# Performance work log

Measured on AMD Instinct MI355X. Metric: run time of the kernel, lower is better.

The kernel has to match this reference:

```python
import jax, jax.numpy as jnp
import numpy as np

B, T, D, H = 2, 2048, 1024, 16
DK = D // H


def setup_inputs() -> dict:
    key = jax.random.key(0)
    ks = jax.random.split(key, 13)
    s = 1.0 / np.sqrt(D)
    return {
        "q": jax.random.normal(ks[0], (B, T, D), jnp.float32),
        "k": jax.random.normal(ks[1], (B, T, D), jnp.float32),
        "v": jax.random.normal(ks[2], (B, T, D), jnp.float32),
        "mask": jax.random.randint(ks[3], (B, T, T), 0, 2, jnp.int32),
        "Wq": jax.random.normal(ks[4], (D, D), jnp.float32) * s,
        "bq": jax.random.normal(ks[5], (D,), jnp.float32) * s,
        "Wk": jax.random.normal(ks[6], (D, D), jnp.float32) * s,
        "bk": jax.random.normal(ks[7], (D,), jnp.float32) * s,
        "Wv": jax.random.normal(ks[8], (D, D), jnp.float32) * s,
        "bv": jax.random.normal(ks[9], (D,), jnp.float32) * s,
        "Wo": jax.random.normal(ks[10], (D, D), jnp.float32) * s,
        "bo": jax.random.normal(ks[11], (D,), jnp.float32) * s,
    }


def reference(q, k, v, mask, Wq, bq, Wk, bk, Wv, bv, Wo, bo):
    # Linear projections (torch Linear: x @ W.T + b), split into heads.
    Q = (q @ Wq.T + bq).reshape(B, T, H, DK).transpose(0, 2, 1, 3)  # [B,H,Tq,dk]
    K = (k @ Wk.T + bk).reshape(B, T, H, DK).transpose(0, 2, 1, 3)
    V = (v @ Wv.T + bv).reshape(B, T, H, DK).transpose(0, 2, 1, 3)
    scores = jnp.einsum("bhqd,bhkd->bhqk", Q, K) / jnp.sqrt(jnp.float32(DK))
    # 3-dim mask path: mask==0 -> -1e9, broadcast over heads.
    scores = jnp.where(mask[:, None, :, :] == 0, jnp.float32(-1e9), scores)
    attn = jax.nn.softmax(scores, axis=-1)
    out = jnp.einsum("bhqk,bhkd->bhqd", attn, V)  # [B,H,Tq,dk]
    out = out.transpose(0, 2, 1, 3).reshape(B, T, D)
    return out @ Wo.T + bo
```

## Files before the change

kernel.cpp:

```cpp
#include <hip/hip_runtime.h>
#include <cstdint>
#include <cstddef>

#define TSEQ 2048
#define DMOD 1024
#define NHEAD 16
#define NBATCH 2
#define MT (NBATCH * TSEQ)
#define LOG2E 1.44269504088896340736f

typedef __attribute__((ext_vector_type(8))) __bf16 bf16x8;
typedef __attribute__((ext_vector_type(4))) float f32x4;
typedef __attribute__((ext_vector_type(8))) unsigned short u16x8;
typedef __attribute__((ext_vector_type(4))) unsigned short u16x4;
typedef __attribute__((ext_vector_type(4))) uint32_t u32x4;

__device__ __forceinline__ unsigned short f2bf(float f) {
  uint32_t u = __builtin_bit_cast(uint32_t, f);
  u += 0x7fffu + ((u >> 16) & 1u);
  return (unsigned short)(u >> 16);
}

__device__ __forceinline__ uint32_t cvt_pk_bf16(float a, float b) {
  uint32_t r;
  asm("v_cvt_pk_bf16_f32 %0, %1, %2" : "=v"(r) : "v"(a), "v"(b));
  return r;
}

__device__ __forceinline__ void gload_lds16(const void* g, const void* l) {
  auto gp = (const __attribute__((address_space(1))) uint32_t*)((uintptr_t)g);
  auto lp = (__attribute__((address_space(3))) uint32_t*)((uintptr_t)l);
  __builtin_amdgcn_global_load_lds(gp, lp, 16, 0, 0);
}

__global__ __launch_bounds__(256) void cvt_all(const float* __restrict__ q,
                                               const float* __restrict__ k,
                                               const float* __restrict__ v,
                                               const float* __restrict__ w0,
                                               const float* __restrict__ w1,
                                               const float* __restrict__ w2,
                                               const float* __restrict__ w3,
                                               unsigned short* __restrict__ din,
                                               unsigned short* __restrict__ dw) {
  const int y = blockIdx.y;
  const float* s;
  unsigned short* d;
  size_t n;
  if (y < 3) {
    s = y == 0 ? q : (y == 1 ? k : v);
    d = din + (size_t)y * MT * DMOD;
    n = (size_t)MT * DMOD;
  } else {
    s = y == 3 ? w0 : (y == 4 ? w1 : (y == 5 ? w2 : w3));
    d = dw + (size_t)(y - 3) * DMOD * DMOD;
    n = (size_t)DMOD * DMOD;
  }
  const size_t i = ((size_t)blockIdx.x * 256 + threadIdx.x) * 4;
  if (i >= n) return;
  const float4 t = *(const float4*)(s + i);
  u16x4 o;
  o[0] = f2bf(t.x); o[1] = f2bf(t.y); o[2] = f2bf(t.z); o[3] = f2bf(t.w);
  *(u16x4*)(d + i) = o;
}

__global__ __launch_bounds__(256) void mask_exp(const int* __restrict__ m,
                                                uint32_t* __restrict__ mx) {
  const size_t W = (size_t)blockIdx.x * 256 + threadIdx.x;
  const int hi = (int)((W >> 3) & 3), ct = (int)(W & 7);
  const size_t bqkt = W >> 5;
  const int kt = (int)(bqkt & 15);
  const size_t bq = bqkt >> 4;
  const int4 mm = *(const int4*)(m + bq * TSEQ + kt * 128 + ct * 16 + hi * 4);
  const uint32_t o = (mm.x ? 0xFFu : 0u) | (mm.y ? 0xFF00u : 0u) |
                     (mm.z ? 0xFF0000u : 0u) | (mm.w ? 0xFF000000u : 0u);
  mx[W] = o;
}

__device__ __forceinline__ void store_c(unsigned short* C, size_t idx, float v) { C[idx] = f2bf(v); }
__device__ __forceinline__ void store_c(float* C, size_t idx, float v) { C[idx] = v; }

template <typename OT, int MF>
__global__ __launch_bounds__(256) void gemm_bt(const unsigned short* __restrict__ A0,
                                               const unsigned short* __restrict__ A1,
                                               const unsigned short* __restrict__ A2,
                                               const unsigned short* __restrict__ W0,
                                               const unsigned short* __restrict__ W1,
                                               const unsigned short* __restrict__ W2,
                                               const float* __restrict__ b0,
                                               const float* __restrict__ b1,
                                               const float* __restrict__ b2,
                                               OT* __restrict__ C0, OT* __restrict__ C1, OT* __restrict__ C2,
                                               float s0, float s1, float s2) {
  constexpr int BM = MF * 32;
  const int z = blockIdx.z;
  const unsigned short* A  = z == 0 ? A0 : (z == 1 ? A1 : A2);
  const unsigned short* Bw = z == 0 ? W0 : (z == 1 ? W1 : W2);
  const float* bias = z == 0 ? b0 : (z == 1 ? b1 : b2);
  OT* C = z == 0 ? C0 : (z == 1 ? C1 : C2);
  const float scale = z == 0 ? s0 : (z == 1 ? s1 : s2);

  __shared__ alignas(16) unsigned short As[BM * 32];
  __shared__ alignas(16) unsigned short Bs[128 * 32];
  const int tid = threadIdx.x;
  const int wid = tid >> 6;
  const int lane = tid & 63;
  const int lo = lane & 15, hi = lane >> 4;
  const int m0 = blockIdx.x * BM, n0 = blockIdx.y * 128;
  const int wr = wid >> 1, wc = wid & 1;
  f32x4 acc[MF][4] = {};

  for (int k0 = 0; k0 < DMOD; k0 += 32) {
    __syncthreads();
#pragma unroll
    for (int i = 0; i < 2; ++i) {
      const int chunk = i * 256 + tid;
      const int row = chunk >> 2, c = chunk & 3;
      const int wb = (i * 256 + wid * 64) * 16;
      if (i < MF / 2)
        gload_lds16(A + (size_t)(m0 + row) * DMOD + k0 + c * 8, (const char*)As + wb);
      gload_lds16(Bw + (size_t)(n0 + row) * DMOD + k0 + c * 8, (const char*)Bs + wb);
    }
    __syncthreads();
    bf16x8 af[MF], bfr[4];
#pragma unroll
    for (int m = 0; m < MF; ++m)
      af[m] = *(const bf16x8*)((const char*)As + (wr * (MF * 16) + m * 16 + lo) * 64 + hi * 16);
#pragma unroll
    for (int n = 0; n < 4; ++n)
      bfr[n] = *(const bf16x8*)((const char*)Bs + (wc * 64 + n * 16 + lo) * 64 + hi * 16);
#pragma unroll
    for (int m = 0; m < MF; ++m)
#pragma unroll
      for (int n = 0; n < 4; ++n)
        acc[m][n] = __builtin_amdgcn_mfma_f32_16x16x32_bf16(af[m], bfr[n], acc[m][n], 0, 0, 0);
  }

#pragma unroll
  for (int n = 0; n < 4; ++n) {
    const int col = n0 + wc * 64 + n * 16 + lo;
    const float bv = bias[col];
#pragma unroll
    for (int m = 0; m < MF; ++m) {
      const int row = m0 + wr * (MF * 16) + m * 16 + hi * 4;
#pragma unroll
      for (int r = 0; r < 4; ++r)
        store_c(C, (size_t)(row + r) * DMOD + col, (acc[m][n][r] + bv) * scale);
    }
  }
}

__global__ __launch_bounds__(256) void transpose_v(const unsigned short* __restrict__ Vp,
                                                   unsigned short* __restrict__ Vt) {
  __shared__ alignas(16) unsigned short tile[64][72];
  const int tid = threadIdx.x;
  const int bt0 = blockIdx.x * 64;
  const int h = blockIdx.y;
  const int b = bt0 >> 11;
  const int t0 = bt0 & (TSEQ - 1);
#pragma unroll
  for (int i = 0; i < 2; ++i) {
    const int chunk = i * 256 + tid;
    const int row = chunk >> 3, c = chunk & 7;
    *(uint4*)((char*)&tile[row][0] + c * 16) =
        *(const uint4*)(Vp + (size_t)(bt0 + row) * DMOD + h * 64 + c * 8);
  }
  __syncthreads();
#pragma unroll
  for (int i = 0; i < 2; ++i) {
    const int chunk = i * 256 + tid;
    const int dk = chunk >> 3, c = chunk & 7;
    u16x8 o;
#pragma unroll
    for (int j = 0; j < 8; ++j) {
      const int x = c * 8 + j;
      const int kl = (x & 32) | ((x & 24) >> 1) | ((x & 4) << 2) | (x & 3);
      o[j] = tile[kl][dk];
    }
    *(u16x8*)(Vt + ((size_t)(b * NHEAD + h) * 64 + dk) * TSEQ + t0 + c * 8) = o;
  }
}

__global__ __launch_bounds__(512, 4) void attn_kernel(const unsigned short* __restrict__ Qp,
                                                      const unsigned short* __restrict__ Kp,
                                                      const unsigned short* __restrict__ Vt,
                                                      const uint32_t* __restrict__ mx,
                                                      unsigned short* __restrict__ AO) {
  __shared__ alignas(16) unsigned short Ks[2][128 * 64];
  __shared__ alignas(16) unsigned short Vs[2][64 * 128];
  const int tid = threadIdx.x;
  const int w = tid >> 6, lane = tid & 63;
  const int lo = lane & 15, hi = lane >> 4;
  const int f = blockIdx.x;
  const int swz = (f & 7) * 64 + (f >> 3);
  const int q0 = (swz & 15) * 128;
  const int h = (swz >> 4) & 15;
  const int b = swz >> 8;

  bf16x8 qf[2];
  {
    const unsigned short* qsrc =
        Qp + (size_t)(b * TSEQ + q0 + w * 16 + lo) * DMOD + h * 64 + hi * 8;
    qf[0] = *(const bf16x8*)qsrc;
    qf[1] = *(const bf16x8*)(qsrc + 32);
  }

  bf16x8 ones;
  {
    u32x4 od;
    od[0] = 0x3F803F80u; od[1] = 0x3F803F80u; od[2] = 0x3F803F80u; od[3] = 0x3F803F80u;
    ones = __builtin_bit_cast(bf16x8, od);
  }

  f32x4 o_acc[4] = {};
  f32x4 l_acc = {};

  const size_t kbase = (size_t)(b * TSEQ) * DMOD + h * 64;
  const size_t vbase = (size_t)(b * NHEAD + h) * 64 * TSEQ;

  const int c0 = tid, c1 = 512 + tid;
  const unsigned short* kp0 = Kp + kbase + (size_t)(c0 >> 3) * DMOD + ((c0 & 7) ^ ((c0 >> 3) & 7)) * 8;
  const unsigned short* kp1 = Kp + kbase + (size_t)(c1 >> 3) * DMOD + ((c1 & 7) ^ ((c1 >> 3) & 7)) * 8;
  const unsigned short* vp0 = Vt + vbase + (size_t)(c0 >> 4) * TSEQ + ((c0 & 15) ^ ((c0 >> 4) & 7)) * 8;
  const unsigned short* vp1 = Vt + vbase + (size_t)(c1 >> 4) * TSEQ + ((c1 & 15) ^ ((c1 >> 4) & 7)) * 8;
  const uint32_t* mp = mx + (size_t)(b * TSEQ + q0 + w * 16 + lo) * 512 + hi * 8;
  const int wb0 = c0 * 16, wb1 = c1 * 16;

  int koffA[8], koffB[8];
#pragma unroll
  for (int ct = 0; ct < 8; ++ct) {
    const int kcol = ct * 16 + lo;
    koffA[ct] = kcol * 128 + ((hi ^ (kcol & 7)) * 16);
    koffB[ct] = kcol * 128 + (((4 + hi) ^ (kcol & 7)) * 16);
  }
  int voff[4][4];
#pragma unroll
  for (int vt = 0; vt < 4; ++vt) {
    const int dk = vt * 16 + lo;
#pragma unroll
    for (int c = 0; c < 4; ++c) voff[vt][c] = dk * 256 + (((c * 4 + hi) ^ (dk & 7)) * 16);
  }

  auto stage = [&](int buf) {
    gload_lds16(kp0, (const char*)Ks[buf] + wb0);
    gload_lds16(kp1, (const char*)Ks[buf] + wb1);
    gload_lds16(vp0, (const char*)Vs[buf] + wb0);
    gload_lds16(vp1, (const char*)Vs[buf] + wb1);
    kp0 += (size_t)128 * DMOD; kp1 += (size_t)128 * DMOD;
    vp0 += 128; vp1 += 128;
  };

  const uint32_t selA = 0x01010000u, selB = 0x03030202u;
  const int NT = TSEQ / 128;

  uint4 mc0 = *(const uint4*)mp, mc1 = *(const uint4*)(mp + 4);
  mp += 32;
  stage(0);
  __syncthreads();

  for (int kt = 0; kt < NT; ++kt) {
    uint4 mn0 = mc0, mn1 = mc1;
    if (kt + 1 < NT) {
      mn0 = *(const uint4*)mp;
      mn1 = *(const uint4*)(mp + 4);
      mp += 32;
      stage((kt + 1) & 1);
    }

    const char* ksb = (const char*)Ks[kt & 1];
    const char* vsb = (const char*)Vs[kt & 1];
    f32x4 s[8];
    __builtin_amdgcn_s_setprio(1);
#pragma unroll
    for (int ct = 0; ct < 8; ++ct) {
      bf16x8 kf0 = *(const bf16x8*)(ksb + koffA[ct]);
      bf16x8 kf1 = *(const bf16x8*)(ksb + koffB[ct]);
      f32x4 zz = {0.f, 0.f, 0.f, 0.f};
      s[ct] = __builtin_amdgcn_mfma_f32_16x16x32_bf16(kf0, qf[0], zz, 0, 0, 0);
      s[ct] = __builtin_amdgcn_mfma_f32_16x16x32_bf16(kf1, qf[1], s[ct], 0, 0, 0);
    }
    __builtin_amdgcn_s_setprio(0);

#pragma unroll
    for (int ct = 0; ct < 8; ++ct) {
      s[ct][0] = __builtin_exp2f(s[ct][0]);
      s[ct][1] = __builtin_exp2f(s[ct][1]);
      s[ct][2] = __builtin_exp2f(s[ct][2]);
      s[ct][3] = __builtin_exp2f(s[ct][3]);
    }

    bf16x8 pf[4];
#pragma unroll
    for (int c = 0; c < 4; ++c) {
      const uint32_t We = c == 0 ? mc0.x : (c == 1 ? mc0.z : (c == 2 ? mc1.x : mc1.z));
      const uint32_t Wo = c == 0 ? mc0.y : (c == 1 ? mc0.w : (c == 2 ? mc1.y : mc1.w));
      u32x4 pd;
      pd[0] = cvt_pk_bf16(s[2 * c][0], s[2 * c][1]) & __builtin_amdgcn_perm(We, We, selA);
      pd[1] = cvt_pk_bf16(s[2 * c][2], s[2 * c][3]) & __builtin_amdgcn_perm(We, We, selB);
      pd[2] = cvt_pk_bf16(s[2 * c + 1][0], s[2 * c + 1][1]) & __builtin_amdgcn_perm(Wo, Wo, selA);
      pd[3] = cvt_pk_bf16(s[2 * c + 1][2], s[2 * c + 1][3]) & __builtin_amdgcn_perm(Wo, Wo, selB);
      pf[c] = __builtin_bit_cast(bf16x8, pd);
    }

    __builtin_amdgcn_s_setprio(1);
#pragma unroll
    for (int vt = 0; vt < 4; ++vt) {
#pragma unroll
      for (int c = 0; c < 4; ++c) {
        bf16x8 vf = *(const bf16x8*)(vsb + voff[vt][c]);
        o_acc[vt] = __builtin_amdgcn_mfma_f32_16x16x32_bf16(pf[c], vf, o_acc[vt], 0, 0, 0);
      }
    }
#pragma unroll
    for (int c = 0; c < 4; ++c)
      l_acc = __builtin_amdgcn_mfma_f32_16x16x32_bf16(pf[c], ones, l_acc, 0, 0, 0);
    __builtin_amdgcn_s_setprio(0);

    __syncthreads();
    mc0 = mn0; mc1 = mn1;
  }

#pragma unroll
  for (int r = 0; r < 4; ++r) {
    const float rl = 1.0f / l_acc[r];
    const size_t orow = (size_t)(b * TSEQ + q0 + w * 16 + hi * 4 + r) * DMOD + h * 64;
#pragma unroll
    for (int vt = 0; vt < 4; ++vt)
      AO[orow + vt * 16 + lo] = f2bf(o_acc[vt][r] * rl);
  }
}

extern "C" void kernel_launch(void* const* d_in, const int* in_sizes, int n_in,
                              void* d_out, int out_size, void* d_ws, size_t ws_size,
                              hipStream_t stream) {
  const float* q  = (const float*)d_in[0];
  const float* k  = (const float*)d_in[1];
  const float* v  = (const float*)d_in[2];
  const int* mask = (const int*)d_in[3];
  const float* Wq = (const float*)d_in[4];
  const float* bq = (const float*)d_in[5];
  const float* Wk = (const float*)d_in[6];
  const float* bk = (const float*)d_in[7];
  const float* Wv = (const float*)d_in[8];
  const float* bv = (const float*)d_in[9];
  const float* Wo = (const float*)d_in[10];
  const float* bo = (const float*)d_in[11];
  float* out = (float*)d_out;

  char* ws = (char*)d_ws;
  const size_t SZ_BT = (size_t)MT * DMOD * 2;
  const size_t SZ_W  = (size_t)DMOD * DMOD * 2;

  unsigned short* qb  = (unsigned short*)(ws + 0);
  unsigned short* kb  = (unsigned short*)(ws + SZ_BT);
  unsigned short* vb  = (unsigned short*)(ws + 2 * SZ_BT);
  unsigned short* Qp  = (unsigned short*)(ws + 3 * SZ_BT);
  unsigned short* Kp  = (unsigned short*)(ws + 4 * SZ_BT);
  unsigned short* Vp  = (unsigned short*)(ws + 5 * SZ_BT);
  unsigned short* Wqb = (unsigned short*)(ws + 6 * SZ_BT);
  unsigned short* Wob = (unsigned short*)(ws + 6 * SZ_BT + 3 * SZ_W);
  unsigned short* Vt  = vb;
  unsigned short* AO  = qb;
  uint32_t*       mx  = (uint32_t*)kb;

  const int nBT = MT * DMOD;
  const int nW  = DMOD * DMOD;

  cvt_all<<<dim3(nBT / 1024, 7), 256, 0, stream>>>(q, k, v, Wq, Wk, Wv, Wo, qb, Wqb);

  const float qs = 0.125f * LOG2E;
  gemm_bt<unsigned short, 4><<<dim3(MT / 128, DMOD / 128, 3), 256, 0, stream>>>(
      qb, kb, vb, Wqb, Wqb + nW, Wqb + 2 * nW, bq, bk, bv, Qp, Kp, Vp, qs, 1.0f, 1.0f);

  mask_exp<<<(NBATCH * TSEQ * 16 * 32) / 256, 256, 0, stream>>>(mask, mx);

  transpose_v<<<dim3(MT / 64, NHEAD), 256, 0, stream>>>(Vp, Vt);

  attn_kernel<<<dim3(512), 512, 0, stream>>>(Qp, Kp, Vt, mx, AO);

  gemm_bt<float, 2><<<dim3(MT / 64, DMOD / 128, 1), 256, 0, stream>>>(
      AO, AO, AO, Wob, Wob, Wob, bo, bo, bo, out, out, out, 1.0f, 1.0f, 1.0f);
}
```

Before: 154.7 us.

## Double-buffer GEMM LDS tiles and swizzle block order across XCDs

```diff
diff --git a/kernel.cpp b/kernel.cpp
--- a/kernel.cpp
+++ b/kernel.cpp
@@ -92,47 +92,64 @@
                                                OT* __restrict__ C0, OT* __restrict__ C1, OT* __restrict__ C2,
                                                float s0, float s1, float s2) {
   constexpr int BM = MF * 32;
-  const int z = blockIdx.z;
+  constexpr int NX = 4096 / BM;
+  const int nb = gridDim.x, per = nb >> 3, bid = blockIdx.x;
+  const int swz = (bid & 7) * per + (bid >> 3);
+  const int z = swz / (NX * 8);
+  const int rem = swz % (NX * 8);
+  const int m0 = (rem >> 3) * BM, n0 = (rem & 7) * 128;
+
   const unsigned short* A  = z == 0 ? A0 : (z == 1 ? A1 : A2);
   const unsigned short* Bw = z == 0 ? W0 : (z == 1 ? W1 : W2);
   const float* bias = z == 0 ? b0 : (z == 1 ? b1 : b2);
   OT* C = z == 0 ? C0 : (z == 1 ? C1 : C2);
   const float scale = z == 0 ? s0 : (z == 1 ? s1 : s2);
 
-  __shared__ alignas(16) unsigned short As[BM * 32];
-  __shared__ alignas(16) unsigned short Bs[128 * 32];
+  __shared__ alignas(16) unsigned short As[2][BM * 32];
+  __shared__ alignas(16) unsigned short Bs[2][128 * 32];
   const int tid = threadIdx.x;
   const int wid = tid >> 6;
   const int lane = tid & 63;
   const int lo = lane & 15, hi = lane >> 4;
-  const int m0 = blockIdx.x * BM, n0 = blockIdx.y * 128;
   const int wr = wid >> 1, wc = wid & 1;
   f32x4 acc[MF][4] = {};
 
-  for (int k0 = 0; k0 < DMOD; k0 += 32) {
-    __syncthreads();
+  const int r0 = tid >> 2, c8 = (tid & 3) * 8;
+  auto stage = [&](int buf, int k0) {
 #pragma unroll
     for (int i = 0; i < 2; ++i) {
       const int chunk = i * 256 + tid;
-      const int row = chunk >> 2, c = chunk & 3;
-      const int wb = (i * 256 + wid * 64) * 16;
       if (i < MF / 2)
-        gload_lds16(A + (size_t)(m0 + row) * DMOD + k0 + c * 8, (const char*)As + wb);
-      gload_lds16(Bw + (size_t)(n0 + row) * DMOD + k0 + c * 8, (const char*)Bs + wb);
-    }
-    __syncthreads();
+        gload_lds16(A + (size_t)(m0 + i * 64 + r0) * DMOD + k0 + c8,
+                    (const char*)As + buf * (BM * 64) + chunk * 16);
+      gload_lds16(Bw + (size_t)(n0 + i * 64 + r0) * DMOD + k0 + c8,
+                  (const char*)Bs + buf * 8192 + chunk * 16);
+    }
+  };
+
+  stage(0, 0);
+  __syncthreads();
+
+  for (int k0 = 0; k0 < DMOD; k0 += 32) {
+    const int cur = (k0 >> 5) & 1;
+    if (k0 + 32 < DMOD) stage(cur ^ 1, k0 + 32);
+
     bf16x8 af[MF], bfr[4];
 #pragma unroll
     for (int m = 0; m < MF; ++m)
-      af[m] = *(const bf16x8*)((const char*)As + (wr * (MF * 16) + m * 16 + lo) * 64 + hi * 16);
+      af[m] = *(const bf16x8*)((const char*)As + cur * (BM * 64) +
+                               (wr * (MF * 16) + m * 16 + lo) * 64 + hi * 16);
 #pragma unroll
     for (int n = 0; n < 4; ++n)
-      bfr[n] = *(const bf16x8*)((const char*)Bs + (wc * 64 + n * 16 + lo) * 64 + hi * 16);
+      bfr[n] = *(const bf16x8*)((const char*)Bs + cur * 8192 +
+                                (wc * 64 + n * 16 + lo) * 64 + hi * 16);
 #pragma unroll
     for (int m = 0; m < MF; ++m)
 #pragma unroll
       for (int n = 0; n < 4; ++n)
         acc[m][n] = __builtin_amdgcn_mfma_f32_16x16x32_bf16(af[m], bfr[n], acc[m][n], 0, 0, 0);
+
+    __syncthreads();
   }
 
 #pragma unroll
@@ -368,7 +385,7 @@
   cvt_all<<<dim3(nBT / 1024, 7), 256, 0, stream>>>(q, k, v, Wq, Wk, Wv, Wo, qb, Wqb);
 
   const float qs = 0.125f * LOG2E;
-  gemm_bt<unsigned short, 4><<<dim3(MT / 128, DMOD / 128, 3), 256, 0, stream>>>(
+  gemm_bt<unsigned short, 4><<<dim3(768), 256, 0, stream>>>(
       qb, kb, vb, Wqb, Wqb + nW, Wqb + 2 * nW, bq, bk, bv, Qp, Kp, Vp, qs, 1.0f, 1.0f);
 
   mask_exp<<<(NBATCH * TSEQ * 16 * 32) / 256, 256, 0, stream>>>(mask, mx);
@@ -377,6 +394,6 @@
 
   attn_kernel<<<dim3(512), 512, 0, stream>>>(Qp, Kp, Vt, mx, AO);
 
-  gemm_bt<float, 2><<<dim3(MT / 64, DMOD / 128, 1), 256, 0, stream>>>(
+  gemm_bt<float, 2><<<dim3(512), 256, 0, stream>>>(
       AO, AO, AO, Wob, Wob, Wob, bo, bo, bo, out, out, out, 1.0f, 1.0f, 1.0f);
 }
```

Result: faster. 148.1 us (-4.3%).
